# Performance work log

Hardware: AMD Instinct MI355X
Metric: run time of the kernel (lower is better)

The kernel has to match this reference:

```python
import jax, jax.numpy as jnp
import numpy as np

VX, VY = 0.2, 0.2
X_OFF = VX / 2 + 0.0      # voxel_size[0]/2 + pc_range[0]
Y_OFF = VY / 2 + (-40.0)  # voxel_size[1]/2 + pc_range[1]
EPS = 1e-3                # BN1d eps from default norm_cfg

N, P, C, UNITS = 40000, 32, 4, 64


def setup_inputs() -> dict:
    key = jax.random.key(0)
    k1, k2, k3, k4 = jax.random.split(key, 4)
    features = jax.random.normal(k1, (N, P, C), dtype=jnp.float32)
    num_voxels = jax.random.randint(k2, (N,), 1, P + 1, dtype=jnp.int32)
    coors = jax.random.randint(k3, (N, 4), 0, 400, dtype=jnp.int32)
    W = jax.random.normal(k4, (UNITS, C + 5), dtype=jnp.float32) * 0.1
    return {
        "features": features,
        "num_voxels": num_voxels,
        "coors": coors,
        "W": W,
        "gamma": jnp.ones((UNITS,), jnp.float32),
        "beta": jnp.zeros((UNITS,), jnp.float32),
        "running_mean": jnp.zeros((UNITS,), jnp.float32),
        "running_var": jnp.ones((UNITS,), jnp.float32),
    }


def reference(features, num_voxels, coors, W, gamma, beta, running_mean, running_var):
    nv = num_voxels.astype(features.dtype)  # [N]
    # cluster offset: point minus mean of valid points (sum over padded zeros / count)
    points_mean = features[:, :, :3].sum(axis=1, keepdims=True) / nv[:, None, None]
    f_cluster = features[:, :, :3] - points_mean  # [N,P,3]
    # center offset (x,y only)
    cx = coors[:, 3].astype(features.dtype) * VX + X_OFF  # [N]
    cy = coors[:, 2].astype(features.dtype) * VY + Y_OFF
    f_center = jnp.stack(
        [features[:, :, 0] - cx[:, None], features[:, :, 1] - cy[:, None]], axis=-1
    )  # [N,P,2]
    feats = jnp.concatenate([features, f_cluster, f_center], axis=-1)  # [N,P,9]
    # zero out padding points
    mask = (num_voxels[:, None] > jnp.arange(P, dtype=num_voxels.dtype)[None, :])
    feats = feats * mask[:, :, None].astype(feats.dtype)
    # PFN layer: linear (no bias) -> BN1d (eval) -> relu -> max over points
    x = jnp.einsum("npc,uc->npu", feats, W)  # [N,P,64]
    x = (x - running_mean) * (gamma * jax.lax.rsqrt(running_var + EPS)) + beta
    x = jax.nn.relu(x)
    x_max = jnp.max(x, axis=1)  # [N,64]
    return x_max
```

## Files before the change

### kernel.cpp

```cpp
#include <hip/hip_runtime.h>
#include <hip/hip_bf16.h>
#include <math.h>


#define NPIL  40000
#define NITER 10
#define WPB   4
#define BLOCK (WPB * 64)
#define NBLK  (NPIL / (WPB * NITER))

typedef float f32x16 __attribute__((ext_vector_type(16)));
typedef short bf16x8 __attribute__((ext_vector_type(8)));

union frag_u { bf16x8 h; int4 w; };

__device__ __forceinline__ int pk(float a, float b) {
    unsigned lo = (unsigned)__bfloat16_as_ushort(__float2bfloat16(a));
    unsigned hi = (unsigned)__bfloat16_as_ushort(__float2bfloat16(b));
    return (int)(lo | (hi << 16));
}
__device__ __forceinline__ float bfround(float x) {
    return __bfloat162float(__float2bfloat16(x));
}

template<int CTRL>
__device__ __forceinline__ float dpp_add(float x) {
    return x + __int_as_float(__builtin_amdgcn_update_dpp(
        0, __float_as_int(x), CTRL, 0xF, 0xF, true));
}
__device__ __forceinline__ float lo32_sum(float x) {
    x = dpp_add<0x111>(x);
    x = dpp_add<0x112>(x);
    x = dpp_add<0x114>(x);
    x = dpp_add<0x118>(x);
    x = dpp_add<0x142>(x);
    return __int_as_float(__builtin_amdgcn_readlane(__float_as_int(x), 31));
}

__device__ __forceinline__ float vmax16(const f32x16& a) {
    float t0 = fmaxf(fmaxf(a[0],  a[1]),  a[2]);
    float t1 = fmaxf(fmaxf(a[3],  a[4]),  a[5]);
    float t2 = fmaxf(fmaxf(a[6],  a[7]),  a[8]);
    float t3 = fmaxf(fmaxf(a[9],  a[10]), a[11]);
    float t4 = fmaxf(fmaxf(a[12], a[13]), a[14]);
    float u0 = fmaxf(fmaxf(t0, t1), t2);
    float u1 = fmaxf(fmaxf(t3, t4), a[15]);
    return fmaxf(u0, u1);
}

__global__ __launch_bounds__(BLOCK, 4)
void pfn_mfma_kernel(const float* __restrict__ features,
                     const int*   __restrict__ num_voxels,
                     const int*   __restrict__ coors,
                     const float* __restrict__ Wm,
                     const float* __restrict__ gamma,
                     const float* __restrict__ beta,
                     const float* __restrict__ rmean,
                     const float* __restrict__ rvar,
                     float* __restrict__ out)
{
    __shared__ int4 sfrag0[64];
    __shared__ int4 sfrag1[64];

    const int  lane = threadIdx.x & 63;
    const int  wid  = threadIdx.x >> 6;
    const int  lo31 = lane & 31;
    const bool hih  = (lane >= 32);

    const int p0 = (blockIdx.x * WPB + wid) * NITER;

    const float* fbase = features + (size_t)p0 * 128 + lo31 * 4;
    float4 qv[NITER];
    #pragma unroll
    for (int j = 0; j < NITER; ++j)
        qv[j] = *reinterpret_cast<const float4*>(fbase + (size_t)j * 128);
    const int  li  = (lane < NITER) ? lane : (NITER - 1);
    const int  nv8 = num_voxels[p0 + li];
    const int2 cc8 = *reinterpret_cast<const int2*>(coors + (p0 + li) * 4 + 2);

    if (wid == 0) {
        #pragma unroll
        for (int t = 0; t < 2; ++t) {
            const int uu = lo31 + t * 32;
            const float* w = Wm + uu * 9;
            const float s  = gamma[uu] * rsqrtf(rvar[uu] + 1e-3f);
            const float tb = beta[uu] - rmean[uu] * s;
            int4 r;
            if (!hih) {
                r.x = pk((w[0] + w[4] + w[7]) * s, (w[1] + w[5] + w[8]) * s);
                r.y = pk((w[2] + w[6]) * s,        w[3] * s);
                r.z = pk(w[4] * s,                 w[5] * s);
                r.w = pk(w[6] * s,                 0.0f);
            } else {
                const float w7s = w[7] * s, w8s = w[8] * s;
                r.x = pk(w7s, w7s);
                r.y = pk(w8s, w8s);
                r.z = pk(tb,  tb - bfround(tb));
                r.w = 0;
            }
            if (t == 0) sfrag0[lane] = r; else sfrag1[lane] = r;
        }
    }
    __syncthreads();

    frag_u bf0, bf1;
    bf0.w = sfrag0[lane];
    bf1.w = sfrag1[lane];

    f32x16 z;
    #pragma unroll
    for (int i = 0; i < 16; ++i) z[i] = 0.0f;

    const int ONE2 = 0x3F803F80;
    const int inv2 = hih ? ONE2 : 0;

    #pragma unroll
    for (int j = 0; j < NITER; ++j) {
        const int   snv = __builtin_amdgcn_readlane(nv8,   j);
        const int   sc2 = __builtin_amdgcn_readlane(cc8.x, j);
        const int   sc3 = __builtin_amdgcn_readlane(cc8.y, j);
        const float4 q  = qv[j];

        const float S0 = lo32_sum(q.x);
        const float S1 = lo32_sum(q.y);
        const float S2 = lo32_sum(q.z);
        const float rn = __builtin_amdgcn_rcpf((float)snv);
        const float cx = (float)sc3 * 0.2f + 0.1f;
        const float cy = (float)sc2 * 0.2f + (0.1f - 40.0f);

        const int f01 = pk(q.x, q.y);
        const int f23 = pk(q.z, q.w);
        const int mxy = pk(-S0 * rn, -S1 * rn);
        const int mz0 = pk(-S2 * rn, 0.0f);
        const int cxw = pk(-cx, -cx - bfround(-cx));
        const int cyw = pk(-cy, -cy - bfround(-cy));

        const bool valid = (lo31 < snv);
        int w0 = hih ? cxw  : f01;  w0 = valid ? w0 : 0;
        int w1 = hih ? cyw  : f23;  w1 = valid ? w1 : 0;
        int w2 = hih ? ONE2 : mxy;  w2 = valid ? w2 : inv2;
        int w3 = hih ? 0    : mz0;  w3 = valid ? w3 : 0;
        frag_u af; af.w = make_int4(w0, w1, w2, w3);

        const f32x16 a0 = __builtin_amdgcn_mfma_f32_32x32x16_bf16(af.h, bf0.h, z, 0, 0, 0);
        const f32x16 a1 = __builtin_amdgcn_mfma_f32_32x32x16_bf16(af.h, bf1.h, z, 0, 0, 0);

        const float m0 = vmax16(a0);
        const float m1 = vmax16(a1);
        const float got  = __shfl_xor(hih ? m0 : m1, 32, 64);
        const float mine = hih ? m1 : m0;
        const float r = fmaxf(fmaxf(mine, got), 0.0f);

        out[(size_t)(p0 + j) * 64 + lane] = r;
    }
}

extern "C" void kernel_launch(void* const* d_in, const int* in_sizes, int n_in,
                              void* d_out, int out_size, void* d_ws, size_t ws_size,
                              hipStream_t stream) {
    const float* features   = (const float*)d_in[0];
    const int*   num_voxels = (const int*)  d_in[1];
    const int*   coors      = (const int*)  d_in[2];
    const float* Wm         = (const float*)d_in[3];
    const float* gamma      = (const float*)d_in[4];
    const float* beta       = (const float*)d_in[5];
    const float* rmean      = (const float*)d_in[6];
    const float* rvar       = (const float*)d_in[7];
    float*       out        = (float*)d_out;

    hipLaunchKernelGGL(pfn_mfma_kernel, dim3(NBLK), dim3(BLOCK), 0, stream,
                       features, num_voxels, coors, Wm, gamma, beta, rmean, rvar, out);
}
```

Baseline: 16.29 us.

## Hoist per-pillar bias terms out of MFMA and halve pillars per wave

The per-pillar terms (cluster mean, pillar center and BN shift) are constant across a pillar's points, so they no longer go into the bf16 MFMA input fragments. Since max(x+B) = max(x) + B, they are folded into a scalar bias applied after the max reduction with fp32 FMAs. Padded points are pushed to a large negative value through a flag column in the B fragment. The result is then clamped with the BN shift when the pillar has padding, which matches the zeroed padded points in the reference. The change also halves pillars per wave (10 to 5) and raises the launch-bounds occupancy hint, giving more blocks and less register pressure at the cost of more block launches.

```diff
diff --git a/kernel.cpp b/kernel.cpp
--- a/kernel.cpp
+++ b/kernel.cpp
@@ -4,7 +4,8 @@
 
 
 #define NPIL  40000
-#define NITER 10
+#define PPTS  32
+#define NITER 5
 #define WPB   4
 #define BLOCK (WPB * 64)
 #define NBLK  (NPIL / (WPB * NITER))
@@ -18,9 +19,6 @@
     unsigned lo = (unsigned)__bfloat16_as_ushort(__float2bfloat16(a));
     unsigned hi = (unsigned)__bfloat16_as_ushort(__float2bfloat16(b));
     return (int)(lo | (hi << 16));
-}
-__device__ __forceinline__ float bfround(float x) {
-    return __bfloat162float(__float2bfloat16(x));
 }
 
 template<int CTRL>
@@ -48,7 +46,7 @@
     return fmaxf(u0, u1);
 }
 
-__global__ __launch_bounds__(BLOCK, 4)
+__global__ __launch_bounds__(BLOCK, 6)
 void pfn_mfma_kernel(const float* __restrict__ features,
                      const int*   __restrict__ num_voxels,
                      const int*   __restrict__ coors,
@@ -59,8 +57,10 @@
                      const float* __restrict__ rvar,
                      float* __restrict__ out)
 {
-    __shared__ int4 sfrag0[64];
-    __shared__ int4 sfrag1[64];
+    __shared__ int4   sB0[64];
+    __shared__ int4   sB1[64];
+    __shared__ float4 sC0[64];
+    __shared__ float2 sC1[64];
 
     const int  lane = threadIdx.x & 63;
     const int  wid  = threadIdx.x >> 6;
@@ -79,40 +79,34 @@
     const int2 cc8 = *reinterpret_cast<const int2*>(coors + (p0 + li) * 4 + 2);
 
     if (wid == 0) {
-        #pragma unroll
-        for (int t = 0; t < 2; ++t) {
-            const int uu = lo31 + t * 32;
-            const float* w = Wm + uu * 9;
-            const float s  = gamma[uu] * rsqrtf(rvar[uu] + 1e-3f);
-            const float tb = beta[uu] - rmean[uu] * s;
-            int4 r;
-            if (!hih) {
-                r.x = pk((w[0] + w[4] + w[7]) * s, (w[1] + w[5] + w[8]) * s);
-                r.y = pk((w[2] + w[6]) * s,        w[3] * s);
-                r.z = pk(w[4] * s,                 w[5] * s);
-                r.w = pk(w[6] * s,                 0.0f);
-            } else {
-                const float w7s = w[7] * s, w8s = w[8] * s;
-                r.x = pk(w7s, w7s);
-                r.y = pk(w8s, w8s);
-                r.z = pk(tb,  tb - bfround(tb));
-                r.w = 0;
-            }
-            if (t == 0) sfrag0[lane] = r; else sfrag1[lane] = r;
-        }
+        const float* w  = Wm + lane * 9;
+        const float  s  = gamma[lane] * rsqrtf(rvar[lane] + 1e-3f);
+        const float  tb = beta[lane] - rmean[lane] * s;
+        int4 mypk;
+        mypk.x = pk((w[0] + w[4] + w[7]) * s, (w[1] + w[5] + w[8]) * s);
+        mypk.y = pk((w[2] + w[6]) * s,        w[3] * s);
+        mypk.z = pk(-1e30f, 0.0f);
+        mypk.w = 0;
+        const int4 zero4 = make_int4(0, 0, 0, 0);
+        if (!hih) { sB0[lane] = mypk;  sB1[lane + 32] = zero4; }
+        else      { sB1[lane - 32] = mypk;  sB0[lane] = zero4; }
+        sC0[lane] = make_float4(w[4] * s, w[5] * s, w[6] * s, tb);
+        sC1[lane] = make_float2(w[7] * s, w[8] * s);
     }
     __syncthreads();
 
     frag_u bf0, bf1;
-    bf0.w = sfrag0[lane];
-    bf1.w = sfrag1[lane];
+    bf0.w = sB0[lane];
+    bf1.w = sB1[lane];
+    const float4 c0 = sC0[lane];
+    const float2 c1 = sC1[lane];
+    const float  tb = c0.w;
 
     f32x16 z;
     #pragma unroll
     for (int i = 0; i < 16; ++i) z[i] = 0.0f;
 
-    const int ONE2 = 0x3F803F80;
-    const int inv2 = hih ? ONE2 : 0;
+    const int flagw = hih ? 0 : 0x3F80;
 
     #pragma unroll
     for (int j = 0; j < NITER; ++j) {
@@ -127,20 +121,21 @@
         const float rn = __builtin_amdgcn_rcpf((float)snv);
         const float cx = (float)sc3 * 0.2f + 0.1f;
         const float cy = (float)sc2 * 0.2f + (0.1f - 40.0f);
+        float B = tb;
+        B = fmaf(-(S0 * rn), c0.x, B);
+        B = fmaf(-(S1 * rn), c0.y, B);
+        B = fmaf(-(S2 * rn), c0.z, B);
+        B = fmaf(-cx, c1.x, B);
+        B = fmaf(-cy, c1.y, B);
 
         const int f01 = pk(q.x, q.y);
         const int f23 = pk(q.z, q.w);
-        const int mxy = pk(-S0 * rn, -S1 * rn);
-        const int mz0 = pk(-S2 * rn, 0.0f);
-        const int cxw = pk(-cx, -cx - bfround(-cx));
-        const int cyw = pk(-cy, -cy - bfround(-cy));
-
-        const bool valid = (lo31 < snv);
-        int w0 = hih ? cxw  : f01;  w0 = valid ? w0 : 0;
-        int w1 = hih ? cyw  : f23;  w1 = valid ? w1 : 0;
-        int w2 = hih ? ONE2 : mxy;  w2 = valid ? w2 : inv2;
-        int w3 = hih ? 0    : mz0;  w3 = valid ? w3 : 0;
-        frag_u af; af.w = make_int4(w0, w1, w2, w3);
+        const bool valid = (lane < snv);
+        frag_u af;
+        af.w = make_int4(valid ? f01 : 0,
+                         valid ? f23 : 0,
+                         valid ? 0 : flagw,
+                         0);
 
         const f32x16 a0 = __builtin_amdgcn_mfma_f32_32x32x16_bf16(af.h, bf0.h, z, 0, 0, 0);
         const f32x16 a1 = __builtin_amdgcn_mfma_f32_32x32x16_bf16(af.h, bf1.h, z, 0, 0, 0);
@@ -149,7 +144,8 @@
         const float m1 = vmax16(a1);
         const float got  = __shfl_xor(hih ? m0 : m1, 32, 64);
         const float mine = hih ? m1 : m0;
-        const float r = fmaxf(fmaxf(mine, got), 0.0f);
+        float r = fmaxf(fmaxf(mine, got) + B, 0.0f);
+        r = fmaxf(r, (snv < PPTS) ? tb : -INFINITY);
 
         out[(size_t)(p0 + j) * 64 + lane] = r;
     }
```

After: 13.92 us (median of 2 runs). -14.5%, faster.
